# Performance work log

Hardware: AMD Instinct MI355X
Metric: run time of the kernel (lower is better)

Reference implementation:

```python
import jax, jax.numpy as jnp
import numpy as np

B, T, I, H = 32768, 50, 2, 32  # batch, seq_len, input_size, hidden_size


def setup_inputs() -> dict:
    key = jax.random.key(0)
    ks = jax.random.split(key, 7)
    return {
        "x": jax.random.normal(ks[0], (B, T, I), dtype=jnp.float32),
        "W_ih": jax.random.normal(ks[1], (4 * H, I), dtype=jnp.float32) * 0.1,
        "W_hh": jax.random.normal(ks[2], (4 * H, H), dtype=jnp.float32) * 0.1,
        "b_ih": jax.random.normal(ks[3], (4 * H,), dtype=jnp.float32) * 0.1,
        "b_hh": jax.random.normal(ks[4], (4 * H,), dtype=jnp.float32) * 0.1,
        "W_out": jax.random.normal(ks[5], (1, H), dtype=jnp.float32) * 0.1,
        "b_out": jax.random.normal(ks[6], (1,), dtype=jnp.float32) * 0.1,
        "h0": jnp.zeros((B, H), dtype=jnp.float32),
        "c0": jnp.zeros((B, H), dtype=jnp.float32),
    }


def reference(x, W_ih, W_hh, b_ih, b_hh, W_out, b_out, h0, c0):
    # Precompute input projection for all timesteps: [B, T, 4H]
    xg = jnp.einsum("bti,gi->btg", x, W_ih) + b_ih + b_hh

    def step(carry, xg_t):
        h, c = carry  # [B, H] each
        gates = xg_t + h @ W_hh.T  # [B, 4H]
        i, f, g, o = jnp.split(gates, 4, axis=-1)  # PyTorch gate order i,f,g,o
        i = jax.nn.sigmoid(i)
        f = jax.nn.sigmoid(f)
        g = jnp.tanh(g)
        o = jax.nn.sigmoid(o)
        c = f * c + i * g
        h = o * jnp.tanh(c)
        return (h, c), h

    (_, _), hs = jax.lax.scan(step, (h0, c0), jnp.swapaxes(xg, 0, 1))  # hs: [T, B, H]
    r_out = jnp.swapaxes(hs, 0, 1)  # [B, T, H]
    results = r_out @ W_out.T + b_out  # [B, T, 1]
    return results.reshape(-1, 50, 1)
```

## Files before the change

### kernel.cpp

```cpp
#include <hip/hip_runtime.h>


#define TS 50
#define HSTR 20
#define CL 14.0f
#define WPB 4

typedef short short8 __attribute__((ext_vector_type(8)));
typedef float f32x4 __attribute__((ext_vector_type(4)));
typedef float f32x2 __attribute__((ext_vector_type(2)));

__device__ __forceinline__ float fast_exp2(float x) {
    return __builtin_amdgcn_exp2f(x);
}
__device__ __forceinline__ float fast_rcp(float x) {
    return __builtin_amdgcn_rcpf(x);
}
__device__ __forceinline__ f32x2 pexp(f32x2 z) {
    f32x2 r; r.x = fast_exp2(z.x); r.y = fast_exp2(z.y); return r;
}
__device__ __forceinline__ f32x2 prcp(f32x2 v) {
    f32x2 r; r.x = fast_rcp(v.x); r.y = fast_rcp(v.y); return r;
}
__device__ __forceinline__ f32x2 vmin2(f32x2 v, float s) {
    f32x2 r; r.x = fminf(v.x, s); r.y = fminf(v.y, s); return r;
}
__device__ __forceinline__ unsigned split_pack(float v) {
    unsigned u   = __float_as_uint(v);
    float    res = v - __uint_as_float(u & 0xffff0000u);
    return __builtin_amdgcn_perm(__float_as_uint(res), u, 0x07060302u);
}
__device__ __forceinline__ unsigned lo_pair(unsigned a, unsigned b) {
    return __builtin_amdgcn_perm(b, a, 0x05040100u);
}
__device__ __forceinline__ unsigned hi_pair(unsigned a, unsigned b) {
    return __builtin_amdgcn_perm(b, a, 0x07060302u);
}

union U4S8 { uint4 v; short8 s; unsigned u[4]; };

__global__ __launch_bounds__(256, 2)
void lsnn_kernel(const float* __restrict__ x,
                 const float* __restrict__ W_ih,
                 const float* __restrict__ W_hh,
                 const float* __restrict__ b_ih,
                 const float* __restrict__ b_hh,
                 const float* __restrict__ W_out,
                 const float* __restrict__ b_out,
                 const float* __restrict__ h0,
                 const float* __restrict__ c0,
                 float* __restrict__ out)
{
    __shared__ __align__(16) float    x_lds[WPB][16 * 100];
    __shared__ __align__(16) unsigned hhi[WPB][16 * HSTR];
    __shared__ __align__(16) unsigned hlo[WPB][16 * HSTR];
    __shared__ __align__(16) float    out_lds[WPB][16 * TS];

    const int  g_w  = threadIdx.x >> 6;
    const int  lane = threadIdx.x & 63;
    const int  u0   = lane & 15;
    const int  q    = lane >> 4;
    const long b0   = ((long)blockIdx.x * WPB + g_w) * 16;

    float*    xw   = x_lds[g_w];
    unsigned* hh_w = hhi[g_w];
    unsigned* hl_w = hlo[g_w];
    float*    ow   = out_lds[g_w];

    {
        const float4* xs = (const float4*)(x + b0 * 100);
        float4* xd = (float4*)xw;
        for (int i = lane; i < 400; i += 64) xd[i] = xs[i];
    }
    for (int i = lane; i < 256; i += 64) {
        int row = i >> 4, j = i & 15;
        float2 v = *(const float2*)&h0[(b0 + row) * 32 + 2 * j];
        unsigned p0 = split_pack(v.x), p1 = split_pack(v.y);
        hh_w[row * HSTR + j] = lo_pair(p0, p1);
        hl_w[row * HSTR + j] = hi_pair(p0, p1);
    }

    const float L2E = 1.4426950408889634f;
    const float SG  = 2.0f * L2E;

    short8 Bh[8], Bl[8], Bx[8];
    #pragma unroll
    for (int n = 0; n < 8; ++n) {
        const float s  = ((n >> 1) == 2) ? SG : -L2E;
        const int   gg = (n >> 1) * 32 + 2 * u0 + (n & 1);
        const float* wr = W_hh + gg * 32 + q * 8;
        U4S8 uh, ul;
        #pragma unroll
        for (int p = 0; p < 4; ++p) {
            unsigned p0 = split_pack(wr[2*p]   * s);
            unsigned p1 = split_pack(wr[2*p+1] * s);
            uh.u[p] = lo_pair(p0, p1);
            ul.u[p] = hi_pair(p0, p1);
        }
        Bh[n] = uh.s;  Bl[n] = ul.s;
        U4S8 ux;
        if (q == 0) {
            unsigned s0 = split_pack(W_ih[gg * 2 + 0] * s);
            unsigned s1 = split_pack(W_ih[gg * 2 + 1] * s);
            unsigned sb = split_pack((b_ih[gg] + b_hh[gg]) * s);
            ux.u[0] = lo_pair(s0, s0);
            ux.u[1] = lo_pair(s1, s1);
            ux.u[2] = hi_pair(s0, s1);
            ux.u[3] = sb;
        } else {
            ux.u[0] = 0u; ux.u[1] = 0u; ux.u[2] = 0u; ux.u[3] = 0u;
        }
        Bx[n] = ux.s;
    }
    short8 Bwh, Bwl;
    {
        U4S8 uh, ul;
        #pragma unroll
        for (int p = 0; p < 4; ++p) {
            unsigned p0 = split_pack(W_out[q * 8 + 2*p]);
            unsigned p1 = split_pack(W_out[q * 8 + 2*p + 1]);
            uh.u[p] = lo_pair(p0, p1);
            ul.u[p] = hi_pair(p0, p1);
        }
        Bwh = uh.s;  Bwl = ul.s;
    }
    const float bout = b_out[0];

    f32x2 cst2[4];
    #pragma unroll
    for (int par = 0; par < 2; ++par)
        #pragma unroll
        for (int rr = 0; rr < 2; ++rr) {
            cst2[par*2+rr].x = c0[(b0 + q*4 + 2*rr    ) * 32 + 2*u0 + par];
            cst2[par*2+rr].y = c0[(b0 + q*4 + 2*rr + 1) * 32 + 2*u0 + par];
        }

    const f32x4 ZV = {0.f, 0.f, 0.f, 0.f};
    const int abase = u0 * HSTR + q * 4;

    float2 xp = *(const float2*)&xw[u0 * 100];

    #pragma unroll 1
    for (int t = 0; t < TS; ++t) {
        U4S8 Ahh, Ahl;
        Ahh.v = *(const uint4*)&hh_w[abase];
        Ahl.v = *(const uint4*)&hl_w[abase];

        if (t > 0) {
            f32x4 aw = ZV;
            aw = __builtin_amdgcn_mfma_f32_16x16x32_bf16(Ahh.s, Bwh, aw, 0, 0, 0);
            aw = __builtin_amdgcn_mfma_f32_16x16x32_bf16(Ahl.s, Bwh, aw, 0, 0, 0);
            aw = __builtin_amdgcn_mfma_f32_16x16x32_bf16(Ahh.s, Bwl, aw, 0, 0, 0);
            if (u0 == 0) {
                #pragma unroll
                for (int r = 0; r < 4; ++r)
                    ow[(q * 4 + r) * TS + (t - 1)] = aw[r] + bout;
            }
        }

        U4S8 Axf;
        {
            unsigned a0 = split_pack(xp.x);
            unsigned a1 = split_pack(xp.y);
            Axf.u[0] = a0;
            Axf.u[1] = a1;
            Axf.u[2] = lo_pair(a0, a1);
            Axf.u[3] = 0x3f803f80u;
        }
        if (t + 1 < TS)
            xp = *(const float2*)&xw[u0 * 100 + 2 * (t + 1)];

        f32x4 acc[8];
        #pragma unroll
        for (int n = 0; n < 8; ++n)
            acc[n] = __builtin_amdgcn_mfma_f32_16x16x32_bf16(Axf.s, Bx[n], ZV, 0, 0, 0);
        #pragma unroll
        for (int n = 0; n < 8; ++n) {
            acc[n] = __builtin_amdgcn_mfma_f32_16x16x32_bf16(Ahh.s, Bh[n], acc[n], 0, 0, 0);
            acc[n] = __builtin_amdgcn_mfma_f32_16x16x32_bf16(Ahl.s, Bh[n], acc[n], 0, 0, 0);
            acc[n] = __builtin_amdgcn_mfma_f32_16x16x32_bf16(Ahh.s, Bl[n], acc[n], 0, 0, 0);
        }

        f32x2 Bv2[4], Cv2[4], P12[4], Ep2[4], PP2[4];
        #pragma unroll
        for (int par = 0; par < 2; ++par) {
            #pragma unroll
            for (int rr = 0; rr < 2; ++rr) {
                const int g = par * 2 + rr;
                f32x2 zi = {acc[0+par][2*rr], acc[0+par][2*rr+1]};
                f32x2 zf = {acc[2+par][2*rr], acc[2+par][2*rr+1]};
                f32x2 zg = vmin2((f32x2){acc[4+par][2*rr], acc[4+par][2*rr+1]}, CL);
                f32x2 zo = {acc[6+par][2*rr], acc[6+par][2*rr+1]};
                f32x2 Av = pexp(zi);
                Bv2[g]   = pexp(zg);
                f32x2 Ev = pexp(zf);
                Cv2[g]   = pexp(zo);
                f32x2 Ap = 1.0f + Av, Bp = 1.0f + Bv2[g];
                Ep2[g] = 1.0f + Ev;
                P12[g] = Ap * Bp;
                PP2[g] = P12[g] * Ep2[g];
            }
        }
        f32x2 R2[4];
        #pragma unroll
        for (int bb = 0; bb < 2; ++bb) {
            f32x2 pr = PP2[2*bb] * PP2[2*bb + 1];
            f32x2 ri = prcp(pr);
            R2[2*bb]     = PP2[2*bb + 1] * ri;
            R2[2*bb + 1] = PP2[2*bb]     * ri;
        }
        f32x2 Dv2[4], Q2[4];
        #pragma unroll
        for (int g = 0; g < 4; ++g) {
            f32x2 fv = P12[g] * R2[g];
            f32x2 ig = (Bv2[g] - 1.0f) * (Ep2[g] * R2[g]);
            f32x2 c  = fv * cst2[g] + ig;
            cst2[g] = c;
            f32x2 zc = vmin2(c * SG, CL);
            Dv2[g] = pexp(zc);
            Q2[g]  = (1.0f + Cv2[g]) * (1.0f + Dv2[g]);
        }
        f32x2 RQ2[4];
        #pragma unroll
        for (int bb = 0; bb < 2; ++bb) {
            f32x2 qr = Q2[2*bb] * Q2[2*bb + 1];
            f32x2 ri = prcp(qr);
            RQ2[2*bb]     = Q2[2*bb + 1] * ri;
            RQ2[2*bb + 1] = Q2[2*bb]     * ri;
        }
        #pragma unroll
        for (int rr = 0; rr < 2; ++rr) {
            f32x2 he = (Dv2[rr]     - 1.0f) * RQ2[rr];
            f32x2 ho = (Dv2[2 + rr] - 1.0f) * RQ2[2 + rr];
            unsigned hex = __float_as_uint(he.x), hey = __float_as_uint(he.y);
            unsigned hox = __float_as_uint(ho.x), hoy = __float_as_uint(ho.y);
            f32x2 rese, reso;
            rese.x = he.x - __uint_as_float(hex & 0xffff0000u);
            rese.y = he.y - __uint_as_float(hey & 0xffff0000u);
            reso.x = ho.x - __uint_as_float(hox & 0xffff0000u);
            reso.y = ho.y - __uint_as_float(hoy & 0xffff0000u);
            const int row0 = q * 4 + 2 * rr;
            hh_w[ row0      * HSTR + u0] = hi_pair(hex, hox);
            hl_w[ row0      * HSTR + u0] = hi_pair(__float_as_uint(rese.x),
                                                   __float_as_uint(reso.x));
            hh_w[(row0 + 1) * HSTR + u0] = hi_pair(hey, hoy);
            hl_w[(row0 + 1) * HSTR + u0] = hi_pair(__float_as_uint(rese.y),
                                                   __float_as_uint(reso.y));
        }
    }

    {
        U4S8 Ahh, Ahl;
        Ahh.v = *(const uint4*)&hh_w[abase];
        Ahl.v = *(const uint4*)&hl_w[abase];
        f32x4 aw = {0.f, 0.f, 0.f, 0.f};
        aw = __builtin_amdgcn_mfma_f32_16x16x32_bf16(Ahh.s, Bwh, aw, 0, 0, 0);
        aw = __builtin_amdgcn_mfma_f32_16x16x32_bf16(Ahl.s, Bwh, aw, 0, 0, 0);
        aw = __builtin_amdgcn_mfma_f32_16x16x32_bf16(Ahh.s, Bwl, aw, 0, 0, 0);
        if (u0 == 0) {
            #pragma unroll
            for (int r = 0; r < 4; ++r)
                ow[(q * 4 + r) * TS + 49] = aw[r] + bout;
        }
    }

    {
        float4* od = (float4*)(out + b0 * 50);
        const float4* os = (const float4*)ow;
        for (int i = lane; i < 200; i += 64) od[i] = os[i];
    }
}

extern "C" void kernel_launch(void* const* d_in, const int* in_sizes, int n_in,
                              void* d_out, int out_size, void* d_ws, size_t ws_size,
                              hipStream_t stream) {
    const float* x     = (const float*)d_in[0];
    const float* W_ih  = (const float*)d_in[1];
    const float* W_hh  = (const float*)d_in[2];
    const float* b_ih  = (const float*)d_in[3];
    const float* b_hh  = (const float*)d_in[4];
    const float* W_out = (const float*)d_in[5];
    const float* b_out = (const float*)d_in[6];
    const float* h0    = (const float*)d_in[7];
    const float* c0    = (const float*)d_in[8];
    float* out = (float*)d_out;

    dim3 grid(32768 / (16 * WPB)), block(64 * WPB);
    lsnn_kernel<<<grid, block, 0, stream>>>(x, W_ih, W_hh, b_ih, b_hh,
                                            W_out, b_out, h0, c0, out);
}
```

Before: 156.4 us.

## Split each 16-row LSTM tile's hidden units across two waves with LDS double buffering

Each block now handles 16 batch rows with two waves, and each wave computes half the hidden units, so its per-step MFMA and gate work is halved and the recurrence's serial latency per step shortens. The new hidden state is exchanged through double-buffered LDS with a __syncthreads every timestep. The x inputs are pre-split into bf16 hi/lo pairs in LDS once up front, and the output projection alternates between the two waves. The cost is a block-wide barrier per step and twice as many waves overall for the same batch.

```diff
diff --git a/kernel.cpp b/kernel.cpp
--- a/kernel.cpp
+++ b/kernel.cpp
@@ -3,8 +3,8 @@
 
 #define TS 50
 #define HSTR 20
+#define XSTR 52
 #define CL 14.0f
-#define WPB 4
 
 typedef short short8 __attribute__((ext_vector_type(8)));
 typedef float f32x4 __attribute__((ext_vector_type(4)));
@@ -39,7 +39,7 @@
 
 union U4S8 { uint4 v; short8 s; unsigned u[4]; };
 
-__global__ __launch_bounds__(256, 2)
+__global__ __launch_bounds__(128, 4)
 void lsnn_kernel(const float* __restrict__ x,
                  const float* __restrict__ W_ih,
                  const float* __restrict__ W_hh,
@@ -51,49 +51,50 @@
                  const float* __restrict__ c0,
                  float* __restrict__ out)
 {
-    __shared__ __align__(16) float    x_lds[WPB][16 * 100];
-    __shared__ __align__(16) unsigned hhi[WPB][16 * HSTR];
-    __shared__ __align__(16) unsigned hlo[WPB][16 * HSTR];
-    __shared__ __align__(16) float    out_lds[WPB][16 * TS];
-
-    const int  g_w  = threadIdx.x >> 6;
-    const int  lane = threadIdx.x & 63;
+    __shared__ __align__(16) unsigned xa0[16 * XSTR];
+    __shared__ __align__(16) unsigned xa1[16 * XSTR];
+    __shared__ __align__(16) unsigned xa2[16 * XSTR];
+    __shared__ __align__(16) unsigned hhi[2][16 * HSTR];
+    __shared__ __align__(16) unsigned hlo[2][16 * HSTR];
+    __shared__ __align__(16) float    ow[16 * TS];
+
+    const int  tid  = threadIdx.x;
+    const int  wv   = tid >> 6;
+    const int  lane = tid & 63;
     const int  u0   = lane & 15;
     const int  q    = lane >> 4;
-    const long b0   = ((long)blockIdx.x * WPB + g_w) * 16;
-
-    float*    xw   = x_lds[g_w];
-    unsigned* hh_w = hhi[g_w];
-    unsigned* hl_w = hlo[g_w];
-    float*    ow   = out_lds[g_w];
-
-    {
-        const float4* xs = (const float4*)(x + b0 * 100);
-        float4* xd = (float4*)xw;
-        for (int i = lane; i < 400; i += 64) xd[i] = xs[i];
-    }
-    for (int i = lane; i < 256; i += 64) {
-        int row = i >> 4, j = i & 15;
-        float2 v = *(const float2*)&h0[(b0 + row) * 32 + 2 * j];
-        unsigned p0 = split_pack(v.x), p1 = split_pack(v.y);
-        hh_w[row * HSTR + j] = lo_pair(p0, p1);
-        hl_w[row * HSTR + j] = hi_pair(p0, p1);
+    const long b0   = (long)blockIdx.x * 16;
+
+    for (int i = tid; i < 800; i += 128) {
+        int row = i / 50, t = i - row * 50;
+        float2 v = *(const float2*)(x + (b0 + row) * 100 + 2 * t);
+        unsigned a0 = split_pack(v.x), a1 = split_pack(v.y);
+        xa0[row * XSTR + t] = a0;
+        xa1[row * XSTR + t] = a1;
+        xa2[row * XSTR + t] = lo_pair(a0, a1);
+    }
+    for (int i = tid; i < 512; i += 128) {
+        int row = i >> 5, u = i & 31;
+        int j = u & 15, half = u >> 4;
+        unsigned p = split_pack(h0[b0 * 32 + i]);
+        ((unsigned short*)&hhi[0][row * HSTR + j])[half] = (unsigned short)(p & 0xffffu);
+        ((unsigned short*)&hlo[0][row * HSTR + j])[half] = (unsigned short)(p >> 16);
     }
 
     const float L2E = 1.4426950408889634f;
     const float SG  = 2.0f * L2E;
 
-    short8 Bh[8], Bl[8], Bx[8];
+    short8 Bh[4], Bl[4], Bx[4];
     #pragma unroll
-    for (int n = 0; n < 8; ++n) {
-        const float s  = ((n >> 1) == 2) ? SG : -L2E;
-        const int   gg = (n >> 1) * 32 + 2 * u0 + (n & 1);
-        const float* wr = W_hh + gg * 32 + q * 8;
+    for (int n = 0; n < 4; ++n) {
+        const float s  = (n == 2) ? SG : -L2E;
+        const int   gg = n * 32 + 16 * wv + u0;
+        const float* wr = W_hh + gg * 32;
         U4S8 uh, ul;
         #pragma unroll
         for (int p = 0; p < 4; ++p) {
-            unsigned p0 = split_pack(wr[2*p]   * s);
-            unsigned p1 = split_pack(wr[2*p+1] * s);
+            unsigned p0 = split_pack(wr[q * 4 + p]      * s);
+            unsigned p1 = split_pack(wr[q * 4 + p + 16] * s);
             uh.u[p] = lo_pair(p0, p1);
             ul.u[p] = hi_pair(p0, p1);
         }
@@ -117,8 +118,8 @@
         U4S8 uh, ul;
         #pragma unroll
         for (int p = 0; p < 4; ++p) {
-            unsigned p0 = split_pack(W_out[q * 8 + 2*p]);
-            unsigned p1 = split_pack(W_out[q * 8 + 2*p + 1]);
+            unsigned p0 = split_pack(W_out[q * 4 + p]);
+            unsigned p1 = split_pack(W_out[q * 4 + p + 16]);
             uh.u[p] = lo_pair(p0, p1);
             ul.u[p] = hi_pair(p0, p1);
         }
@@ -126,27 +127,32 @@
     }
     const float bout = b_out[0];
 
-    f32x2 cst2[4];
+    f32x2 cst2[2];
     #pragma unroll
-    for (int par = 0; par < 2; ++par)
-        #pragma unroll
-        for (int rr = 0; rr < 2; ++rr) {
-            cst2[par*2+rr].x = c0[(b0 + q*4 + 2*rr    ) * 32 + 2*u0 + par];
-            cst2[par*2+rr].y = c0[(b0 + q*4 + 2*rr + 1) * 32 + 2*u0 + par];
-        }
+    for (int rr = 0; rr < 2; ++rr) {
+        cst2[rr].x = c0[(b0 + q * 4 + 2 * rr    ) * 32 + 16 * wv + u0];
+        cst2[rr].y = c0[(b0 + q * 4 + 2 * rr + 1) * 32 + 16 * wv + u0];
+    }
+
+    __syncthreads();
 
     const f32x4 ZV = {0.f, 0.f, 0.f, 0.f};
     const int abase = u0 * HSTR + q * 4;
-
-    float2 xp = *(const float2*)&xw[u0 * 100];
+    int cur = 0;
 
     #pragma unroll 1
     for (int t = 0; t < TS; ++t) {
         U4S8 Ahh, Ahl;
-        Ahh.v = *(const uint4*)&hh_w[abase];
-        Ahl.v = *(const uint4*)&hl_w[abase];
-
-        if (t > 0) {
+        Ahh.v = *(const uint4*)&hhi[cur][abase];
+        Ahl.v = *(const uint4*)&hlo[cur][abase];
+
+        U4S8 Axf;
+        Axf.u[0] = xa0[u0 * XSTR + t];
+        Axf.u[1] = xa1[u0 * XSTR + t];
+        Axf.u[2] = xa2[u0 * XSTR + t];
+        Axf.u[3] = 0x3f803f80u;
+
+        if (t > 0 && (t & 1) == wv) {
             f32x4 aw = ZV;
             aw = __builtin_amdgcn_mfma_f32_16x16x32_bf16(Ahh.s, Bwh, aw, 0, 0, 0);
             aw = __builtin_amdgcn_mfma_f32_16x16x32_bf16(Ahl.s, Bwh, aw, 0, 0, 0);
@@ -158,101 +164,79 @@
             }
         }
 
-        U4S8 Axf;
-        {
-            unsigned a0 = split_pack(xp.x);
-            unsigned a1 = split_pack(xp.y);
-            Axf.u[0] = a0;
-            Axf.u[1] = a1;
-            Axf.u[2] = lo_pair(a0, a1);
-            Axf.u[3] = 0x3f803f80u;
-        }
-        if (t + 1 < TS)
-            xp = *(const float2*)&xw[u0 * 100 + 2 * (t + 1)];
-
-        f32x4 acc[8];
-        #pragma unroll
-        for (int n = 0; n < 8; ++n)
+        f32x4 acc[4];
+        #pragma unroll
+        for (int n = 0; n < 4; ++n)
             acc[n] = __builtin_amdgcn_mfma_f32_16x16x32_bf16(Axf.s, Bx[n], ZV, 0, 0, 0);
         #pragma unroll
-        for (int n = 0; n < 8; ++n) {
+        for (int n = 0; n < 4; ++n) {
             acc[n] = __builtin_amdgcn_mfma_f32_16x16x32_bf16(Ahh.s, Bh[n], acc[n], 0, 0, 0);
             acc[n] = __builtin_amdgcn_mfma_f32_16x16x32_bf16(Ahl.s, Bh[n], acc[n], 0, 0, 0);
             acc[n] = __builtin_amdgcn_mfma_f32_16x16x32_bf16(Ahh.s, Bl[n], acc[n], 0, 0, 0);
         }
 
-        f32x2 Bv2[4], Cv2[4], P12[4], Ep2[4], PP2[4];
-        #pragma unroll
-        for (int par = 0; par < 2; ++par) {
+        f32x2 Bv2[2], Cv2[2], P12[2], Ep2[2], PP2[2];
+        #pragma unroll
+        for (int rr = 0; rr < 2; ++rr) {
+            f32x2 zi = {acc[0][2*rr], acc[0][2*rr+1]};
+            f32x2 zf = {acc[1][2*rr], acc[1][2*rr+1]};
+            f32x2 zg = vmin2((f32x2){acc[2][2*rr], acc[2][2*rr+1]}, CL);
+            f32x2 zo = {acc[3][2*rr], acc[3][2*rr+1]};
+            f32x2 Av = pexp(zi);
+            Bv2[rr]  = pexp(zg);
+            f32x2 Ev = pexp(zf);
+            Cv2[rr]  = pexp(zo);
+            f32x2 Ap = 1.0f + Av, Bp = 1.0f + Bv2[rr];
+            Ep2[rr] = 1.0f + Ev;
+            P12[rr] = Ap * Bp;
+            PP2[rr] = P12[rr] * Ep2[rr];
+        }
+        f32x2 R2[2];
+        {
+            f32x2 pr = PP2[0] * PP2[1];
+            f32x2 ri = prcp(pr);
+            R2[0] = PP2[1] * ri;
+            R2[1] = PP2[0] * ri;
+        }
+        f32x2 Dv2[2], Q2[2];
+        #pragma unroll
+        for (int rr = 0; rr < 2; ++rr) {
+            f32x2 fv = P12[rr] * R2[rr];
+            f32x2 ig = (Bv2[rr] - 1.0f) * (Ep2[rr] * R2[rr]);
+            f32x2 c  = fv * cst2[rr] + ig;
+            cst2[rr] = c;
+            f32x2 zc = vmin2(c * SG, CL);
+            Dv2[rr] = pexp(zc);
+            Q2[rr]  = (1.0f + Cv2[rr]) * (1.0f + Dv2[rr]);
+        }
+        f32x2 RQ2[2];
+        {
+            f32x2 qr = Q2[0] * Q2[1];
+            f32x2 ri = prcp(qr);
+            RQ2[0] = Q2[1] * ri;
+            RQ2[1] = Q2[0] * ri;
+        }
+        #pragma unroll
+        for (int rr = 0; rr < 2; ++rr) {
+            f32x2 h2 = (Dv2[rr] - 1.0f) * RQ2[rr];
             #pragma unroll
-            for (int rr = 0; rr < 2; ++rr) {
-                const int g = par * 2 + rr;
-                f32x2 zi = {acc[0+par][2*rr], acc[0+par][2*rr+1]};
-                f32x2 zf = {acc[2+par][2*rr], acc[2+par][2*rr+1]};
-                f32x2 zg = vmin2((f32x2){acc[4+par][2*rr], acc[4+par][2*rr+1]}, CL);
-                f32x2 zo = {acc[6+par][2*rr], acc[6+par][2*rr+1]};
-                f32x2 Av = pexp(zi);
-                Bv2[g]   = pexp(zg);
-                f32x2 Ev = pexp(zf);
-                Cv2[g]   = pexp(zo);
-                f32x2 Ap = 1.0f + Av, Bp = 1.0f + Bv2[g];
-                Ep2[g] = 1.0f + Ev;
-                P12[g] = Ap * Bp;
-                PP2[g] = P12[g] * Ep2[g];
+            for (int e = 0; e < 2; ++e) {
+                float hv = e ? h2.y : h2.x;
+                unsigned u   = __float_as_uint(hv);
+                unsigned res = __float_as_uint(hv - __uint_as_float(u & 0xffff0000u));
+                const int row = q * 4 + 2 * rr + e;
+                ((unsigned short*)&hhi[cur ^ 1][row * HSTR + u0])[wv] = (unsigned short)(u >> 16);
+                ((unsigned short*)&hlo[cur ^ 1][row * HSTR + u0])[wv] = (unsigned short)(res >> 16);
             }
         }
-        f32x2 R2[4];
-        #pragma unroll
-        for (int bb = 0; bb < 2; ++bb) {
-            f32x2 pr = PP2[2*bb] * PP2[2*bb + 1];
-            f32x2 ri = prcp(pr);
-            R2[2*bb]     = PP2[2*bb + 1] * ri;
-            R2[2*bb + 1] = PP2[2*bb]     * ri;
-        }
-        f32x2 Dv2[4], Q2[4];
-        #pragma unroll
-        for (int g = 0; g < 4; ++g) {
-            f32x2 fv = P12[g] * R2[g];
-            f32x2 ig = (Bv2[g] - 1.0f) * (Ep2[g] * R2[g]);
-            f32x2 c  = fv * cst2[g] + ig;
-            cst2[g] = c;
-            f32x2 zc = vmin2(c * SG, CL);
-            Dv2[g] = pexp(zc);
-            Q2[g]  = (1.0f + Cv2[g]) * (1.0f + Dv2[g]);
-        }
-        f32x2 RQ2[4];
-        #pragma unroll
-        for (int bb = 0; bb < 2; ++bb) {
-            f32x2 qr = Q2[2*bb] * Q2[2*bb + 1];
-            f32x2 ri = prcp(qr);
-            RQ2[2*bb]     = Q2[2*bb + 1] * ri;
-            RQ2[2*bb + 1] = Q2[2*bb]     * ri;
-        }
-        #pragma unroll
-        for (int rr = 0; rr < 2; ++rr) {
-            f32x2 he = (Dv2[rr]     - 1.0f) * RQ2[rr];
-            f32x2 ho = (Dv2[2 + rr] - 1.0f) * RQ2[2 + rr];
-            unsigned hex = __float_as_uint(he.x), hey = __float_as_uint(he.y);
-            unsigned hox = __float_as_uint(ho.x), hoy = __float_as_uint(ho.y);
-            f32x2 rese, reso;
-            rese.x = he.x - __uint_as_float(hex & 0xffff0000u);
-            rese.y = he.y - __uint_as_float(hey & 0xffff0000u);
-            reso.x = ho.x - __uint_as_float(hox & 0xffff0000u);
-            reso.y = ho.y - __uint_as_float(hoy & 0xffff0000u);
-            const int row0 = q * 4 + 2 * rr;
-            hh_w[ row0      * HSTR + u0] = hi_pair(hex, hox);
-            hl_w[ row0      * HSTR + u0] = hi_pair(__float_as_uint(rese.x),
-                                                   __float_as_uint(reso.x));
-            hh_w[(row0 + 1) * HSTR + u0] = hi_pair(hey, hoy);
-            hl_w[(row0 + 1) * HSTR + u0] = hi_pair(__float_as_uint(rese.y),
-                                                   __float_as_uint(reso.y));
-        }
-    }
-
-    {
+        __syncthreads();
+        cur ^= 1;
+    }
+
+    if (wv == 0) {
         U4S8 Ahh, Ahl;
-        Ahh.v = *(const uint4*)&hh_w[abase];
-        Ahl.v = *(const uint4*)&hl_w[abase];
+        Ahh.v = *(const uint4*)&hhi[cur][abase];
+        Ahl.v = *(const uint4*)&hlo[cur][abase];
         f32x4 aw = {0.f, 0.f, 0.f, 0.f};
         aw = __builtin_amdgcn_mfma_f32_16x16x32_bf16(Ahh.s, Bwh, aw, 0, 0, 0);
         aw = __builtin_amdgcn_mfma_f32_16x16x32_bf16(Ahl.s, Bwh, aw, 0, 0, 0);
@@ -263,11 +247,12 @@
                 ow[(q * 4 + r) * TS + 49] = aw[r] + bout;
         }
     }
+    __syncthreads();
 
     {
         float4* od = (float4*)(out + b0 * 50);
         const float4* os = (const float4*)ow;
-        for (int i = lane; i < 200; i += 64) od[i] = os[i];
+        for (int i = tid; i < 200; i += 128) od[i] = os[i];
     }
 }
 
@@ -285,7 +270,7 @@
     const float* c0    = (const float*)d_in[8];
     float* out = (float*)d_out;
 
-    dim3 grid(32768 / (16 * WPB)), block(64 * WPB);
+    dim3 grid(32768 / 16), block(128);
     lsnn_kernel<<<grid, block, 0, stream>>>(x, W_ih, W_hh, b_ih, b_hh,
                                             W_out, b_out, h0, c0, out);
 }
```

Result: slower. 161.4 us (+3.2%).

## Transpose recurrent MFMA so hidden state stays in registers, skip LDS round-trip

Applied to the files above, without the earlier changes.

Swaps the MFMA operand roles so weights are the A operand and the hidden state is the B operand. Each lane's h outputs then land exactly where the next step's B fragment needs them, so h is repacked in registers with v_cvt_pk_bf16_f32 instead of being written to and re-read from LDS every timestep. The x input is pre-split into bf16 hi/lo words once at load time into padded LDS arrays, removing per-step conversion. This removes per-step LDS stores, loads and the wait on them from the serial recurrence, at the cost of inline asm and a different rounding path for the bf16 split.

```diff
diff --git a/kernel.cpp b/kernel.cpp
--- a/kernel.cpp
+++ b/kernel.cpp
@@ -2,7 +2,7 @@
 
 
 #define TS 50
-#define HSTR 20
+#define XSTR 51
 #define CL 14.0f
 #define WPB 4
 
@@ -35,6 +35,15 @@
 }
 __device__ __forceinline__ unsigned hi_pair(unsigned a, unsigned b) {
     return __builtin_amdgcn_perm(b, a, 0x07060302u);
+}
+__device__ __forceinline__ void pack2(float a, float b,
+                                      unsigned &whi, unsigned &wlo) {
+    unsigned h, l;
+    asm("v_cvt_pk_bf16_f32 %0, %1, %2" : "=v"(h) : "v"(a), "v"(b));
+    float ra = a - __uint_as_float(h << 16);
+    float rb = b - __uint_as_float(h & 0xffff0000u);
+    asm("v_cvt_pk_bf16_f32 %0, %1, %2" : "=v"(l) : "v"(ra), "v"(rb));
+    whi = h; wlo = l;
 }
 
 union U4S8 { uint4 v; short8 s; unsigned u[4]; };
@@ -51,58 +60,56 @@
                  const float* __restrict__ c0,
                  float* __restrict__ out)
 {
-    __shared__ __align__(16) float    x_lds[WPB][16 * 100];
-    __shared__ __align__(16) unsigned hhi[WPB][16 * HSTR];
-    __shared__ __align__(16) unsigned hlo[WPB][16 * HSTR];
+    __shared__ __align__(16) unsigned xa0[WPB][16 * XSTR];
+    __shared__ __align__(16) unsigned xa1[WPB][16 * XSTR];
+    __shared__ __align__(16) unsigned xa2[WPB][16 * XSTR];
     __shared__ __align__(16) float    out_lds[WPB][16 * TS];
 
-    const int  g_w  = threadIdx.x >> 6;
-    const int  lane = threadIdx.x & 63;
+    const int  tid  = threadIdx.x;
+    const int  g_w  = tid >> 6;
+    const int  lane = tid & 63;
     const int  u0   = lane & 15;
     const int  q    = lane >> 4;
     const long b0   = ((long)blockIdx.x * WPB + g_w) * 16;
 
-    float*    xw   = x_lds[g_w];
-    unsigned* hh_w = hhi[g_w];
-    unsigned* hl_w = hlo[g_w];
-    float*    ow   = out_lds[g_w];
-
-    {
-        const float4* xs = (const float4*)(x + b0 * 100);
-        float4* xd = (float4*)xw;
-        for (int i = lane; i < 400; i += 64) xd[i] = xs[i];
-    }
-    for (int i = lane; i < 256; i += 64) {
-        int row = i >> 4, j = i & 15;
-        float2 v = *(const float2*)&h0[(b0 + row) * 32 + 2 * j];
-        unsigned p0 = split_pack(v.x), p1 = split_pack(v.y);
-        hh_w[row * HSTR + j] = lo_pair(p0, p1);
-        hl_w[row * HSTR + j] = hi_pair(p0, p1);
+    unsigned* x0w = xa0[g_w];
+    unsigned* x1w = xa1[g_w];
+    unsigned* x2w = xa2[g_w];
+    float*    ow  = out_lds[g_w];
+
+    for (int i = lane; i < 800; i += 64) {
+        int row = i / 50, t = i - row * 50;
+        float2 v = *(const float2*)(x + (b0 + row) * 100 + 2 * t);
+        unsigned a0 = split_pack(v.x), a1 = split_pack(v.y);
+        x0w[row * XSTR + t] = a0;
+        x1w[row * XSTR + t] = a1;
+        x2w[row * XSTR + t] = lo_pair(a0, a1);
     }
 
     const float L2E = 1.4426950408889634f;
     const float SG  = 2.0f * L2E;
 
-    short8 Bh[8], Bl[8], Bx[8];
+    short8 Awh[8], Awl[8], Aci[8];
     #pragma unroll
     for (int n = 0; n < 8; ++n) {
-        const float s  = ((n >> 1) == 2) ? SG : -L2E;
-        const int   gg = (n >> 1) * 32 + 2 * u0 + (n & 1);
-        const float* wr = W_hh + gg * 32 + q * 8;
+        const int   g  = n & 3, ub = n >> 2;
+        const float s  = (g == 2) ? SG : -L2E;
+        const int   R  = g * 32 + ub * 16 + u0;
+        const float* wr = W_hh + R * 32;
         U4S8 uh, ul;
         #pragma unroll
         for (int p = 0; p < 4; ++p) {
-            unsigned p0 = split_pack(wr[2*p]   * s);
-            unsigned p1 = split_pack(wr[2*p+1] * s);
+            unsigned p0 = split_pack(wr[q * 4 + p]      * s);
+            unsigned p1 = split_pack(wr[q * 4 + p + 16] * s);
             uh.u[p] = lo_pair(p0, p1);
             ul.u[p] = hi_pair(p0, p1);
         }
-        Bh[n] = uh.s;  Bl[n] = ul.s;
+        Awh[n] = uh.s;  Awl[n] = ul.s;
         U4S8 ux;
         if (q == 0) {
-            unsigned s0 = split_pack(W_ih[gg * 2 + 0] * s);
-            unsigned s1 = split_pack(W_ih[gg * 2 + 1] * s);
-            unsigned sb = split_pack((b_ih[gg] + b_hh[gg]) * s);
+            unsigned s0 = split_pack(W_ih[R * 2 + 0] * s);
+            unsigned s1 = split_pack(W_ih[R * 2 + 1] * s);
+            unsigned sb = split_pack((b_ih[R] + b_hh[R]) * s);
             ux.u[0] = lo_pair(s0, s0);
             ux.u[1] = lo_pair(s1, s1);
             ux.u[2] = hi_pair(s0, s1);
@@ -110,95 +117,93 @@
         } else {
             ux.u[0] = 0u; ux.u[1] = 0u; ux.u[2] = 0u; ux.u[3] = 0u;
         }
-        Bx[n] = ux.s;
-    }
-    short8 Bwh, Bwl;
+        Aci[n] = ux.s;
+    }
+    short8 Awoh, Awol;
     {
         U4S8 uh, ul;
         #pragma unroll
         for (int p = 0; p < 4; ++p) {
-            unsigned p0 = split_pack(W_out[q * 8 + 2*p]);
-            unsigned p1 = split_pack(W_out[q * 8 + 2*p + 1]);
+            unsigned p0 = split_pack(W_out[q * 4 + p]);
+            unsigned p1 = split_pack(W_out[q * 4 + p + 16]);
             uh.u[p] = lo_pair(p0, p1);
             ul.u[p] = hi_pair(p0, p1);
         }
-        Bwh = uh.s;  Bwl = ul.s;
+        Awoh = uh.s;  Awol = ul.s;
     }
     const float bout = b_out[0];
 
+    U4S8 Bhh, Bhl;
+    {
+        const float* hp = h0 + (b0 + u0) * 32 + q * 4;
+        float4 ha = *(const float4*)hp;
+        float4 hb = *(const float4*)(hp + 16);
+        pack2(ha.x, hb.x, Bhh.u[0], Bhl.u[0]);
+        pack2(ha.y, hb.y, Bhh.u[1], Bhl.u[1]);
+        pack2(ha.z, hb.z, Bhh.u[2], Bhl.u[2]);
+        pack2(ha.w, hb.w, Bhh.u[3], Bhl.u[3]);
+    }
     f32x2 cst2[4];
     #pragma unroll
-    for (int par = 0; par < 2; ++par)
-        #pragma unroll
-        for (int rr = 0; rr < 2; ++rr) {
-            cst2[par*2+rr].x = c0[(b0 + q*4 + 2*rr    ) * 32 + 2*u0 + par];
-            cst2[par*2+rr].y = c0[(b0 + q*4 + 2*rr + 1) * 32 + 2*u0 + par];
-        }
+    for (int ub = 0; ub < 2; ++ub)
+        #pragma unroll
+        for (int rr = 0; rr < 2; ++rr)
+            cst2[ub * 2 + rr] =
+                *(const f32x2*)(c0 + (b0 + u0) * 32 + ub * 16 + q * 4 + 2 * rr);
 
     const f32x4 ZV = {0.f, 0.f, 0.f, 0.f};
-    const int abase = u0 * HSTR + q * 4;
-
-    float2 xp = *(const float2*)&xw[u0 * 100];
+    const int xbase = u0 * XSTR;
+
+    unsigned xw0 = x0w[xbase], xw1 = x1w[xbase], xw2 = x2w[xbase];
 
     #pragma unroll 1
     for (int t = 0; t < TS; ++t) {
-        U4S8 Ahh, Ahl;
-        Ahh.v = *(const uint4*)&hh_w[abase];
-        Ahl.v = *(const uint4*)&hl_w[abase];
+        U4S8 Bx;
+        Bx.u[0] = xw0;  Bx.u[1] = xw1;  Bx.u[2] = xw2;
+        Bx.u[3] = 0x3f803f80u;
+        if (t + 1 < TS) {
+            xw0 = x0w[xbase + t + 1];
+            xw1 = x1w[xbase + t + 1];
+            xw2 = x2w[xbase + t + 1];
+        }
 
         if (t > 0) {
             f32x4 aw = ZV;
-            aw = __builtin_amdgcn_mfma_f32_16x16x32_bf16(Ahh.s, Bwh, aw, 0, 0, 0);
-            aw = __builtin_amdgcn_mfma_f32_16x16x32_bf16(Ahl.s, Bwh, aw, 0, 0, 0);
-            aw = __builtin_amdgcn_mfma_f32_16x16x32_bf16(Ahh.s, Bwl, aw, 0, 0, 0);
-            if (u0 == 0) {
-                #pragma unroll
-                for (int r = 0; r < 4; ++r)
-                    ow[(q * 4 + r) * TS + (t - 1)] = aw[r] + bout;
-            }
-        }
-
-        U4S8 Axf;
-        {
-            unsigned a0 = split_pack(xp.x);
-            unsigned a1 = split_pack(xp.y);
-            Axf.u[0] = a0;
-            Axf.u[1] = a1;
-            Axf.u[2] = lo_pair(a0, a1);
-            Axf.u[3] = 0x3f803f80u;
-        }
-        if (t + 1 < TS)
-            xp = *(const float2*)&xw[u0 * 100 + 2 * (t + 1)];
+            aw = __builtin_amdgcn_mfma_f32_16x16x32_bf16(Awoh, Bhh.s, aw, 0, 0, 0);
+            aw = __builtin_amdgcn_mfma_f32_16x16x32_bf16(Awoh, Bhl.s, aw, 0, 0, 0);
+            aw = __builtin_amdgcn_mfma_f32_16x16x32_bf16(Awol, Bhh.s, aw, 0, 0, 0);
+            if (q == 0) ow[u0 * TS + (t - 1)] = aw[0] + bout;
+        }
 
         f32x4 acc[8];
         #pragma unroll
         for (int n = 0; n < 8; ++n)
-            acc[n] = __builtin_amdgcn_mfma_f32_16x16x32_bf16(Axf.s, Bx[n], ZV, 0, 0, 0);
+            acc[n] = __builtin_amdgcn_mfma_f32_16x16x32_bf16(Aci[n], Bx.s, ZV, 0, 0, 0);
         #pragma unroll
         for (int n = 0; n < 8; ++n) {
-            acc[n] = __builtin_amdgcn_mfma_f32_16x16x32_bf16(Ahh.s, Bh[n], acc[n], 0, 0, 0);
-            acc[n] = __builtin_amdgcn_mfma_f32_16x16x32_bf16(Ahl.s, Bh[n], acc[n], 0, 0, 0);
-            acc[n] = __builtin_amdgcn_mfma_f32_16x16x32_bf16(Ahh.s, Bl[n], acc[n], 0, 0, 0);
+            acc[n] = __builtin_amdgcn_mfma_f32_16x16x32_bf16(Awh[n], Bhh.s, acc[n], 0, 0, 0);
+            acc[n] = __builtin_amdgcn_mfma_f32_16x16x32_bf16(Awh[n], Bhl.s, acc[n], 0, 0, 0);
+            acc[n] = __builtin_amdgcn_mfma_f32_16x16x32_bf16(Awl[n], Bhh.s, acc[n], 0, 0, 0);
         }
 
         f32x2 Bv2[4], Cv2[4], P12[4], Ep2[4], PP2[4];
         #pragma unroll
-        for (int par = 0; par < 2; ++par) {
+        for (int ub = 0; ub < 2; ++ub) {
             #pragma unroll
             for (int rr = 0; rr < 2; ++rr) {
-                const int g = par * 2 + rr;
-                f32x2 zi = {acc[0+par][2*rr], acc[0+par][2*rr+1]};
-                f32x2 zf = {acc[2+par][2*rr], acc[2+par][2*rr+1]};
-                f32x2 zg = vmin2((f32x2){acc[4+par][2*rr], acc[4+par][2*rr+1]}, CL);
-                f32x2 zo = {acc[6+par][2*rr], acc[6+par][2*rr+1]};
+                const int gi = ub * 2 + rr, nb = ub * 4;
+                f32x2 zi = {acc[nb + 0][2*rr], acc[nb + 0][2*rr + 1]};
+                f32x2 zf = {acc[nb + 1][2*rr], acc[nb + 1][2*rr + 1]};
+                f32x2 zg = vmin2((f32x2){acc[nb + 2][2*rr], acc[nb + 2][2*rr + 1]}, CL);
+                f32x2 zo = {acc[nb + 3][2*rr], acc[nb + 3][2*rr + 1]};
                 f32x2 Av = pexp(zi);
-                Bv2[g]   = pexp(zg);
+                Bv2[gi]  = pexp(zg);
                 f32x2 Ev = pexp(zf);
-                Cv2[g]   = pexp(zo);
-                f32x2 Ap = 1.0f + Av, Bp = 1.0f + Bv2[g];
-                Ep2[g] = 1.0f + Ev;
-                P12[g] = Ap * Bp;
-                PP2[g] = P12[g] * Ep2[g];
+                Cv2[gi]  = pexp(zo);
+                f32x2 Ap = 1.0f + Av, Bp = 1.0f + Bv2[gi];
+                Ep2[gi] = 1.0f + Ev;
+                P12[gi] = Ap * Bp;
+                PP2[gi] = P12[gi] * Ep2[gi];
             }
         }
         f32x2 R2[4];
@@ -211,14 +216,14 @@
         }
         f32x2 Dv2[4], Q2[4];
         #pragma unroll
-        for (int g = 0; g < 4; ++g) {
-            f32x2 fv = P12[g] * R2[g];
-            f32x2 ig = (Bv2[g] - 1.0f) * (Ep2[g] * R2[g]);
-            f32x2 c  = fv * cst2[g] + ig;
-            cst2[g] = c;
+        for (int gi = 0; gi < 4; ++gi) {
+            f32x2 fv = P12[gi] * R2[gi];
+            f32x2 ig = (Bv2[gi] - 1.0f) * (Ep2[gi] * R2[gi]);
+            f32x2 c  = fv * cst2[gi] + ig;
+            cst2[gi] = c;
             f32x2 zc = vmin2(c * SG, CL);
-            Dv2[g] = pexp(zc);
-            Q2[g]  = (1.0f + Cv2[g]) * (1.0f + Dv2[g]);
+            Dv2[gi] = pexp(zc);
+            Q2[gi]  = (1.0f + Cv2[gi]) * (1.0f + Dv2[gi]);
         }
         f32x2 RQ2[4];
         #pragma unroll
@@ -228,40 +233,24 @@
             RQ2[2*bb]     = Q2[2*bb + 1] * ri;
             RQ2[2*bb + 1] = Q2[2*bb]     * ri;
         }
-        #pragma unroll
-        for (int rr = 0; rr < 2; ++rr) {
-            f32x2 he = (Dv2[rr]     - 1.0f) * RQ2[rr];
-            f32x2 ho = (Dv2[2 + rr] - 1.0f) * RQ2[2 + rr];
-            unsigned hex = __float_as_uint(he.x), hey = __float_as_uint(he.y);
-            unsigned hox = __float_as_uint(ho.x), hoy = __float_as_uint(ho.y);
-            f32x2 rese, reso;
-            rese.x = he.x - __uint_as_float(hex & 0xffff0000u);
-            rese.y = he.y - __uint_as_float(hey & 0xffff0000u);
-            reso.x = ho.x - __uint_as_float(hox & 0xffff0000u);
-            reso.y = ho.y - __uint_as_float(hoy & 0xffff0000u);
-            const int row0 = q * 4 + 2 * rr;
-            hh_w[ row0      * HSTR + u0] = hi_pair(hex, hox);
-            hl_w[ row0      * HSTR + u0] = hi_pair(__float_as_uint(rese.x),
-                                                   __float_as_uint(reso.x));
-            hh_w[(row0 + 1) * HSTR + u0] = hi_pair(hey, hoy);
-            hl_w[(row0 + 1) * HSTR + u0] = hi_pair(__float_as_uint(rese.y),
-                                                   __float_as_uint(reso.y));
-        }
-    }
-
-    {
-        U4S8 Ahh, Ahl;
-        Ahh.v = *(const uint4*)&hh_w[abase];
-        Ahl.v = *(const uint4*)&hl_w[abase];
+        float hub[2][4];
+        #pragma unroll
+        for (int gi = 0; gi < 4; ++gi) {
+            f32x2 h2 = (Dv2[gi] - 1.0f) * RQ2[gi];
+            hub[gi >> 1][2 * (gi & 1)]     = h2.x;
+            hub[gi >> 1][2 * (gi & 1) + 1] = h2.y;
+        }
+        #pragma unroll
+        for (int p = 0; p < 4; ++p)
+            pack2(hub[0][p], hub[1][p], Bhh.u[p], Bhl.u[p]);
+    }
+
+    {
         f32x4 aw = {0.f, 0.f, 0.f, 0.f};
-        aw = __builtin_amdgcn_mfma_f32_16x16x32_bf16(Ahh.s, Bwh, aw, 0, 0, 0);
-        aw = __builtin_amdgcn_mfma_f32_16x16x32_bf16(Ahl.s, Bwh, aw, 0, 0, 0);
-        aw = __builtin_amdgcn_mfma_f32_16x16x32_bf16(Ahh.s, Bwl, aw, 0, 0, 0);
-        if (u0 == 0) {
-            #pragma unroll
-            for (int r = 0; r < 4; ++r)
-                ow[(q * 4 + r) * TS + 49] = aw[r] + bout;
-        }
+        aw = __builtin_amdgcn_mfma_f32_16x16x32_bf16(Awoh, Bhh.s, aw, 0, 0, 0);
+        aw = __builtin_amdgcn_mfma_f32_16x16x32_bf16(Awoh, Bhl.s, aw, 0, 0, 0);
+        aw = __builtin_amdgcn_mfma_f32_16x16x32_bf16(Awol, Bhh.s, aw, 0, 0, 0);
+        if (q == 0) ow[u0 * TS + 49] = aw[0] + bout;
     }
 
     {
```

Result: no change. 153.4 us (-1.9%).
